# Performance work log

Measured on AMD Instinct MI355X. Metric: run time of the kernel, lower is better.

## Reference

```python
import jax, jax.numpy as jnp
import numpy as np

S, D = 4096, 512


def setup_inputs() -> dict:
    key = jax.random.key(0)
    ks = jax.random.split(key, 10)
    names = ['x', 'w_ql', 'w_kl', 'w_qr', 'w_kr', 'w_qg', 'w_kg', 'w_qloc', 'w_kloc', 'w_v']
    shapes = [(S, D)] + [(D, D)] * 9
    scale = [1.0] + [float(np.sqrt(2.0 / (D + D)))] * 9  # xavier-ish for weights
    return {n: jax.random.normal(k, sh, dtype=jnp.float32) * s
            for n, k, sh, s in zip(names, ks, shapes, scale)}


def reference(x, w_ql, w_kl, w_qr, w_kr, w_qg, w_kg, w_qloc, w_kloc, w_v):
    # x: [S, D]
    s, d = x.shape
    norm = jnp.sqrt(jnp.asarray(d, x.dtype))
    # strict upper triangle (j > i) is masked for the left boundary,
    # strict lower triangle (i > j) for the right boundary
    mask_up = jnp.triu(jnp.ones((s, s), dtype=bool), k=1)

    ql, kl = x @ w_ql, x @ w_kl
    qr, kr = x @ w_qr, x @ w_kr

    neg_inf = jnp.asarray(-jnp.inf, x.dtype)
    left_scores = jnp.where(mask_up, neg_inf, ql @ kl.T) / norm            # [S,S]
    left_boundary = jax.nn.softmax(left_scores, axis=1)
    right_scores = jnp.where(mask_up.T, neg_inf, qr @ kr.T) / norm
    right_boundary = jax.nn.softmax(right_scores, axis=1)

    # left_boundary @ triu(ones)  == forward cumsum along columns
    # right_boundary @ tril(ones) == reverse cumsum along columns
    left_cdf = jnp.cumsum(left_boundary, axis=1)
    right_cdf = jnp.cumsum(right_boundary[:, ::-1], axis=1)[:, ::-1]
    att_mask = left_cdf * right_cdf                                        # [S,S]

    s_glb = (x @ w_qg) @ (x @ w_kg).T                                      # [S,S]
    s_loc = ((x @ w_qloc) @ (x @ w_kloc).T) * att_mask                     # additive local path
    score = (s_glb + s_loc) / norm

    att_weight = jax.nn.softmax(score, axis=1)
    att_output = att_weight @ (x @ w_v)                                    # [S,D]
    return att_output, att_weight
```

## Files before the change

kernel.cpp:

```cpp
#include <hip/hip_runtime.h>


#define SS 4096
#define DD 512
#define INV_NORM 0.04419417382415922f

typedef _Float16 f16;
typedef f16 f16x8 __attribute__((ext_vector_type(8)));
typedef f16 f16x4 __attribute__((ext_vector_type(4)));
typedef float f32x4 __attribute__((ext_vector_type(4)));
typedef unsigned short ushort;
typedef ushort ushort4v __attribute__((ext_vector_type(4)));

#define GAS __attribute__((address_space(1)))
#define LAS __attribute__((address_space(3)))

#define BARM() asm volatile("s_barrier" ::: "memory")
#define WAITV(N) asm volatile("s_waitcnt vmcnt(" #N ")" ::: "memory")

__device__ __forceinline__ void ldsdma16(const void* g, void* l) {
  __builtin_amdgcn_global_load_lds((const GAS void*)g, (LAS void*)l, 16, 0, 0);
}

__device__ __forceinline__ ushort f2bf(float f) {
  unsigned u = __float_as_uint(f);
  return (ushort)((u + 0x7FFFu + ((u >> 16) & 1u)) >> 16);
}
__device__ __forceinline__ float bf2f(ushort h) {
  return __uint_as_float((unsigned)h << 16);
}

__device__ __forceinline__ void stage16(const f16* __restrict__ src, int ldk, f16* lds, int k0) {
  const int tid  = threadIdx.x;
  const int lane = tid & 63;
  const int wv   = tid >> 6;
  const int rb   = wv * 8 + (lane >> 3);
  const int cs   = lane & 7;
#pragma unroll
  for (int c = 0; c < 4; ++c) {
    const int r = c * 32 + rb;
    const int q = cs ^ (r & 7);
    ldsdma16(src + (size_t)r * ldk + k0 + q * 8, lds + c * 2048 + wv * 512);
  }
}

__device__ __forceinline__ f16x8 fragld(const f16* lds, int r0, int qb) {
  const int lane = threadIdx.x & 63;
  const int r = r0 + (lane & 15);
  const int q = (qb + (lane >> 4)) ^ (r & 7);
  return *(const f16x8*)(lds + r * 64 + q * 8);
}

__device__ __forceinline__ void mma64(const f16* As, const f16* Bs, f32x4 acc[2][8]) {
  const int wv = threadIdx.x >> 6;
#pragma unroll
  for (int ks = 0; ks < 2; ++ks) {
    const f16x8 a0 = fragld(As, wv * 32,      ks * 4);
    const f16x8 a1 = fragld(As, wv * 32 + 16, ks * 4);
#pragma unroll
    for (int j = 0; j < 8; ++j) {
      const f16x8 b = fragld(Bs, j * 16, ks * 4);
      acc[0][j] = __builtin_amdgcn_mfma_f32_16x16x32_f16(a0, b, acc[0][j], 0, 0, 0);
      acc[1][j] = __builtin_amdgcn_mfma_f32_16x16x32_f16(a1, b, acc[1][j], 0, 0, 0);
    }
  }
}

__global__ void k_cvt_x(const float* __restrict__ x, f16* __restrict__ xh) {
  const size_t i = ((size_t)blockIdx.x * 256 + threadIdx.x) * 4;
  const float4 f = *(const float4*)(x + i);
  f16x4 h = { (f16)f.x, (f16)f.y, (f16)f.z, (f16)f.w };
  *(f16x4*)(xh + i) = h;
}

__global__ void k_trw(const float* w0, const float* w1, const float* w2, const float* w3,
                      const float* w4, const float* w5, const float* w6, const float* w7,
                      const float* w8, f16* __restrict__ wt) {
  const float* srcs[9] = {w0, w1, w2, w3, w4, w5, w6, w7, w8};
  const float* src = srcs[blockIdx.z];
  f16* dst = wt + (size_t)blockIdx.z * DD * DD;
  __shared__ float t[32][33];
  const int n0 = blockIdx.x * 32, k0 = blockIdx.y * 32;
  const int tx = threadIdx.x, ty = threadIdx.y;
#pragma unroll
  for (int i = 0; i < 32; i += 8)
    t[ty + i][tx] = src[(size_t)(k0 + ty + i) * DD + n0 + tx];
  __syncthreads();
#pragma unroll
  for (int i = 0; i < 32; i += 8)
    dst[(size_t)(n0 + ty + i) * DD + k0 + tx] = (f16)t[tx][ty + i];
}

__global__ void k_trv(const f16* __restrict__ v, f16* __restrict__ vt) {
  __shared__ f16 t[32][33];
  const int n0 = blockIdx.x * 32, s0 = blockIdx.y * 32;
  const int tx = threadIdx.x, ty = threadIdx.y;
#pragma unroll
  for (int i = 0; i < 32; i += 8)
    t[ty + i][tx] = v[(size_t)(s0 + ty + i) * DD + n0 + tx];
  __syncthreads();
#pragma unroll
  for (int i = 0; i < 32; i += 8)
    vt[(size_t)(n0 + ty + i) * SS + s0 + tx] = t[tx][ty + i];
}

__global__ __launch_bounds__(256, 3) void k_proj(const f16* __restrict__ xh,
                                                 const f16* __restrict__ wt,
                                                 f16* __restrict__ proj) {
  __shared__ __align__(16) f16 As[8192];
  __shared__ __align__(16) f16 Bs[8192];
  const int z = blockIdx.z;
  const f16* B = wt + (size_t)z * DD * DD;
  f16* C = proj + (size_t)z * SS * DD;
  const int R0 = blockIdx.y * 128, C0 = blockIdx.x * 128;
  f32x4 acc[2][8];
#pragma unroll
  for (int i = 0; i < 2; ++i)
#pragma unroll
    for (int j = 0; j < 8; ++j) acc[i][j] = (f32x4){0.f, 0.f, 0.f, 0.f};
  for (int kb = 0; kb < DD / 64; ++kb) {
    __syncthreads();
    stage16(xh + (size_t)R0 * DD, DD, As, kb * 64);
    stage16(B  + (size_t)C0 * DD, DD, Bs, kb * 64);
    __syncthreads();
    mma64(As, Bs, acc);
  }
  const int lane = threadIdx.x & 63, wv = threadIdx.x >> 6;
  const int mm = lane & 15, quad = lane >> 4;
#pragma unroll
  for (int i = 0; i < 2; ++i)
#pragma unroll
    for (int j = 0; j < 8; ++j)
#pragma unroll
      for (int r = 0; r < 4; ++r)
        C[(size_t)(R0 + wv * 32 + i * 16 + quad * 4 + r) * DD + C0 + j * 16 + mm] =
            (f16)acc[i][j][r];
}

__global__ __launch_bounds__(256, 3) void k_bnd(const f16* __restrict__ proj,
                                                f16* __restrict__ eL,
                                                f16* __restrict__ eR) {
  const int t = blockIdx.x, dir = blockIdx.y;
  int rbk = (int)((sqrtf(8.f * t + 1.f) - 1.f) * 0.5f);
  while ((rbk + 1) * (rbk + 2) / 2 <= t) ++rbk;
  while (rbk * (rbk + 1) / 2 > t) --rbk;
  int jt = t - rbk * (rbk + 1) / 2;
  if (dir) { jt = 31 - jt; rbk = 31 - rbk; }
  __shared__ __align__(16) f16 As[8192];
  __shared__ __align__(16) f16 Bs[8192];
  const f16* q  = proj + (size_t)(dir ? 2 : 0) * SS * DD;
  const f16* kp = proj + (size_t)(dir ? 3 : 1) * SS * DD;
  const int R0 = rbk * 128, C0 = jt * 128;
  f32x4 acc[2][8];
#pragma unroll
  for (int i = 0; i < 2; ++i)
#pragma unroll
    for (int j = 0; j < 8; ++j) acc[i][j] = (f32x4){0.f, 0.f, 0.f, 0.f};
  for (int kb = 0; kb < DD / 64; ++kb) {
    __syncthreads();
    stage16(q  + (size_t)R0 * DD, DD, As, kb * 64);
    stage16(kp + (size_t)C0 * DD, DD, Bs, kb * 64);
    __syncthreads();
    mma64(As, Bs, acc);
  }
  const int lane = threadIdx.x & 63, wv = threadIdx.x >> 6;
  const int mm = lane & 15, quad = lane >> 4;
  const bool diag = (jt == rbk);
  f16* outp = dir ? eR : eL;
#pragma unroll
  for (int i = 0; i < 2; ++i)
#pragma unroll
    for (int r = 0; r < 4; ++r) {
      const int rl = wv * 32 + i * 16 + quad * 4 + r;
#pragma unroll
      for (int j = 0; j < 8; ++j) {
        const int cl = j * 16 + mm;
        const float sc = acc[i][j][r] * INV_NORM;
        const bool bad = diag && (dir ? (cl < rl) : (cl > rl));
        const float e = bad ? 0.f : __expf(sc);
        outp[(size_t)(R0 + rl) * SS + (C0 + cl)] = (f16)e;
      }
    }
}

__global__ __launch_bounds__(1024) void k_cumsum(f16* __restrict__ eL,
                                                 const f16* __restrict__ eR) {
  const int i = blockIdx.x;
  const int tid = threadIdx.x, lane = tid & 63, wv = tid >> 6;
  __shared__ float wsL[16], wsR[16];
  const int j0 = tid * 4;

  float pl[4] = {0.f, 0.f, 0.f, 0.f};
  if (j0 <= i) {
    const f16x4 hl = *(const f16x4*)(eL + (size_t)i * SS + j0);
#pragma unroll
    for (int u = 0; u < 4; ++u) pl[u] = (j0 + u <= i) ? (float)hl[u] : 0.f;
  }
#pragma unroll
  for (int u = 1; u < 4; ++u) pl[u] += pl[u - 1];
  const float Tl = pl[3];
  float sl = Tl;
#pragma unroll
  for (int d = 1; d < 64; d <<= 1) {
    const float o = __shfl_up(sl, (unsigned)d, 64);
    if (lane >= d) sl += o;
  }
  if (lane == 63) wsL[wv] = sl;

  float rr[4] = {0.f, 0.f, 0.f, 0.f}, pr[4];
  if (j0 + 3 >= i) {
    const f16x4 hr = *(const f16x4*)(eR + (size_t)i * SS + j0);
#pragma unroll
    for (int u = 0; u < 4; ++u) rr[u] = (j0 + u >= i) ? (float)hr[u] : 0.f;
  }
  pr[0] = rr[0];
#pragma unroll
  for (int u = 1; u < 4; ++u) pr[u] = pr[u - 1] + rr[u];
  const float Tr = pr[3];
  float sr = Tr;
#pragma unroll
  for (int d = 1; d < 64; d <<= 1) {
    const float o = __shfl_up(sr, (unsigned)d, 64);
    if (lane >= d) sr += o;
  }
  if (lane == 63) wsR[wv] = sr;

  __syncthreads();
  float offL = 0.f, totL = 0.f, offR = 0.f, totR = 0.f;
#pragma unroll
  for (int ww = 0; ww < 16; ++ww) {
    const float a = wsL[ww], b = wsR[ww];
    if (ww < wv) { offL += a; offR += b; }
    totL += a; totR += b;
  }
  const float exL = offL + sl - Tl;
  const float exR = offR + sr - Tr;
  const float invL = 1.f / totL, invR = 1.f / totR;

  f16x4 out;
#pragma unroll
  for (int u = 0; u < 4; ++u) {
    const int j = j0 + u;
    const float cdfL = (exL + pl[u]) * invL;
    const float pre  = exR + pr[u];
    const float cdfR = (totR - pre + rr[u]) * invR;
    const float m = (j < i) ? cdfL : ((j > i) ? cdfR : 1.f);
    out[u] = (f16)m;
  }
  *(f16x4*)(eL + (size_t)i * SS + j0) = out;
}

__device__ __forceinline__ float mask_ld(const f16* Am, const f16* Bm, int r, int c) {
  const f16* b = (c < 64) ? Am : Bm;
  const int cc = c & 63;
  const int q = (cc >> 3) ^ (r & 7);
  return (float)b[r * 64 + q * 8 + (cc & 7)];
}

__global__ __launch_bounds__(256, 2) void k_score(const f16* __restrict__ proj,
                                                  const f16* __restrict__ mask,
                                                  f16* __restrict__ ehalf,
                                                  float* __restrict__ lsc) {
  __shared__ __align__(16) f16 Ag[8192];
  __shared__ __align__(16) f16 Bg[8192];
  __shared__ __align__(16) f16 Al[8192];
  __shared__ __align__(16) f16 Bl[8192];
  const int jt = blockIdx.x, rbk = blockIdx.y;
  const f16* qg = proj + (size_t)4 * SS * DD;
  const f16* kg = proj + (size_t)5 * SS * DD;
  const f16* ql = proj + (size_t)6 * SS * DD;
  const f16* kl = proj + (size_t)7 * SS * DD;
  const int R0 = rbk * 128, C0 = jt * 128;
  f32x4 ag[2][8], al[2][8];
#pragma unroll
  for (int i = 0; i < 2; ++i)
#pragma unroll
    for (int j = 0; j < 8; ++j) {
      ag[i][j] = (f32x4){0.f, 0.f, 0.f, 0.f};
      al[i][j] = (f32x4){0.f, 0.f, 0.f, 0.f};
    }
  stage16(qg + (size_t)R0 * DD, DD, Ag, 0);
  stage16(kg + (size_t)C0 * DD, DD, Bg, 0);
  stage16(ql + (size_t)R0 * DD, DD, Al, 0);
  stage16(kl + (size_t)C0 * DD, DD, Bl, 0);
  for (int kb = 0; kb < DD / 64 - 1; ++kb) {
    WAITV(8);
    BARM();
    mma64(Ag, Bg, ag);
    BARM();
    stage16(qg + (size_t)R0 * DD, DD, Ag, kb * 64 + 64);
    stage16(kg + (size_t)C0 * DD, DD, Bg, kb * 64 + 64);
    WAITV(8);
    BARM();
    mma64(Al, Bl, al);
    BARM();
    stage16(ql + (size_t)R0 * DD, DD, Al, kb * 64 + 64);
    stage16(kl + (size_t)C0 * DD, DD, Bl, kb * 64 + 64);
  }
  WAITV(8);
  BARM();
  mma64(Ag, Bg, ag);
  BARM();
  stage16(mask + (size_t)R0 * SS, SS, Ag, C0);
  stage16(mask + (size_t)R0 * SS, SS, Bg, C0 + 64);
  WAITV(16);
  BARM();
  mma64(Al, Bl, al);
  WAITV(0);
  BARM();

  const int lane = threadIdx.x & 63, wv = threadIdx.x >> 6;
  const int mm = lane & 15, quad = lane >> 4;
  float ls[2][4];
#pragma unroll
  for (int i = 0; i < 2; ++i)
#pragma unroll
    for (int r = 0; r < 4; ++r) ls[i][r] = 0.f;
#pragma unroll
  for (int i = 0; i < 2; ++i)
#pragma unroll
    for (int r = 0; r < 4; ++r) {
      const int rl = wv * 32 + i * 16 + quad * 4 + r;
      const int rg = R0 + rl;
#pragma unroll
      for (int j = 0; j < 8; ++j) {
        const int cl = j * 16 + mm;
        const float mk = mask_ld(Ag, Bg, rl, cl);
        const float scv = (ag[i][j][r] + al[i][j][r] * mk) * INV_NORM;
        const float e = __expf(scv);
        ehalf[(size_t)rg * SS + (C0 + cl)] = (f16)e;
        ls[i][r] += e;
      }
    }
#pragma unroll
  for (int d = 1; d < 16; d <<= 1)
#pragma unroll
    for (int i = 0; i < 2; ++i)
#pragma unroll
      for (int r = 0; r < 4; ++r)
        ls[i][r] += __shfl_xor(ls[i][r], d, 64);
  if (mm == 0) {
#pragma unroll
    for (int i = 0; i < 2; ++i)
#pragma unroll
      for (int r = 0; r < 4; ++r)
        atomicAdd(&lsc[R0 + wv * 32 + i * 16 + quad * 4 + r], ls[i][r]);
  }
}

__global__ __launch_bounds__(256, 4) void k_pv(const f16* __restrict__ ehalf,
                                               const f16* __restrict__ vt,
                                               ushort* __restrict__ part) {
  __shared__ __align__(16) f16 As[8192];
  __shared__ __align__(16) f16 Bs[8192];
  const int C0 = blockIdx.x * 128, R0 = blockIdx.y * 128, zk = blockIdx.z;
  f32x4 acc[2][8];
#pragma unroll
  for (int i = 0; i < 2; ++i)
#pragma unroll
    for (int j = 0; j < 8; ++j) acc[i][j] = (f32x4){0.f, 0.f, 0.f, 0.f};
  for (int kb = 0; kb < 16; ++kb) {
    const int k0 = zk * 1024 + kb * 64;
    __syncthreads();
    stage16(ehalf + (size_t)R0 * SS, SS, As, k0);
    stage16(vt    + (size_t)C0 * SS, SS, Bs, k0);
    __syncthreads();
    mma64(As, Bs, acc);
  }
  const int lane = threadIdx.x & 63, wv = threadIdx.x >> 6;
  const int mm = lane & 15, quad = lane >> 4;
  ushort* P = part + (size_t)zk * SS * DD;
#pragma unroll
  for (int i = 0; i < 2; ++i)
#pragma unroll
    for (int j = 0; j < 8; ++j)
#pragma unroll
      for (int r = 0; r < 4; ++r)
        P[(size_t)(R0 + wv * 32 + i * 16 + quad * 4 + r) * DD + C0 + j * 16 + mm] =
            f2bf(acc[i][j][r]);
}

__global__ void k_fin(const f16* __restrict__ ehalf, const ushort* __restrict__ part,
                      const float* __restrict__ lsc, float* __restrict__ outw,
                      float* __restrict__ O) {
  const int bx = blockIdx.x;
  if (bx < 8192) {
    const size_t idx = ((size_t)bx * 256 + threadIdx.x) * 8;
    const int row = (int)(idx >> 12);
    const float inv = 1.f / lsc[row];
    const f16x8 h = *(const f16x8*)(ehalf + idx);
    float4 a = { (float)h[0] * inv, (float)h[1] * inv, (float)h[2] * inv, (float)h[3] * inv };
    float4 b = { (float)h[4] * inv, (float)h[5] * inv, (float)h[6] * inv, (float)h[7] * inv };
    *(float4*)(outw + idx) = a;
    *(float4*)(outw + idx + 4) = b;
  } else {
    const size_t idx = ((size_t)(bx - 8192) * 256 + threadIdx.x) * 4;
    const int row = (int)(idx >> 9);
    float s0 = 0.f, s1 = 0.f, s2 = 0.f, s3 = 0.f;
#pragma unroll
    for (int p = 0; p < 4; ++p) {
      const ushort4v v = *(const ushort4v*)(part + (size_t)p * SS * DD + idx);
      s0 += bf2f(v[0]); s1 += bf2f(v[1]); s2 += bf2f(v[2]); s3 += bf2f(v[3]);
    }
    const float inv = 1.f / lsc[row];
    float4 s = { s0 * inv, s1 * inv, s2 * inv, s3 * inv };
    *(float4*)(O + idx) = s;
  }
}

extern "C" void kernel_launch(void* const* d_in, const int* in_sizes, int n_in,
                              void* d_out, int out_size, void* d_ws, size_t ws_size,
                              hipStream_t stream) {
  (void)in_sizes; (void)n_in; (void)out_size; (void)ws_size;
  const float* x = (const float*)d_in[0];
  const float* w[9];
  for (int i = 0; i < 9; ++i) w[i] = (const float*)d_in[1 + i];
  float* O    = (float*)d_out;
  float* outw = O + (size_t)SS * DD;

  char* ws = (char*)d_ws;
  size_t off = 0;
  auto alloc = [&](size_t b) { void* p = ws + off; off += (b + 255) & ~(size_t)255; return p; };
  f16* xh     = (f16*)alloc((size_t)SS * DD * 2);
  f16* wt     = (f16*)alloc((size_t)9 * DD * DD * 2);
  f16* proj   = (f16*)alloc((size_t)9 * SS * DD * 2);
  f16* vt     = (f16*)alloc((size_t)DD * SS * 2);
  f16* eL     = (f16*)alloc((size_t)SS * SS * 2);
  f16* eR     = (f16*)alloc((size_t)SS * SS * 2);
  f16* ehalf  = (f16*)alloc((size_t)SS * SS * 2);
  float* lsc  = (float*)alloc((size_t)SS * 4);
  ushort* part = (ushort*)eR;

  hipMemsetAsync(lsc, 0, (size_t)SS * 4, stream);
  k_cvt_x<<<SS * DD / 1024, 256, 0, stream>>>(x, xh);
  k_trw<<<dim3(16, 16, 9), dim3(32, 8), 0, stream>>>(w[0], w[1], w[2], w[3], w[4],
                                                     w[5], w[6], w[7], w[8], wt);
  k_proj<<<dim3(4, 32, 9), 256, 0, stream>>>(xh, wt, proj);
  k_trv<<<dim3(16, 128), dim3(32, 8), 0, stream>>>(proj + (size_t)8 * SS * DD, vt);
  k_bnd<<<dim3(528, 2), 256, 0, stream>>>(proj, eL, eR);
  k_cumsum<<<SS, 1024, 0, stream>>>(eL, eR);
  k_score<<<dim3(32, 32), 256, 0, stream>>>(proj, eL, ehalf, lsc);
  k_pv<<<dim3(4, 32, 4), 256, 0, stream>>>(ehalf, vt, part);
  k_fin<<<10240, 256, 0, stream>>>(ehalf, part, lsc, outw, O);
}
```

Before: 290.6 us.

## Swizzle score block order, raise MFMA priority, halve PV column tile

The score kernel now remaps block indices so that consecutive workgroups land in different row and column tiles, aiming for better L2 reuse across XCDs. It raises wave priority around the MFMA sections and fixes the vmcnt wait before the last local-path MMA. The PV kernel moves from 128-column to 64-column tiles with a half-size B stage and a narrower MMA, doubling the grid for more parallelism. The narrower tile means each loaded ehalf tile is reused across fewer output columns, so A-side traffic rises.

```diff
diff --git a/kernel.cpp b/kernel.cpp
--- a/kernel.cpp
+++ b/kernel.cpp
@@ -44,6 +44,20 @@
   }
 }
 
+__device__ __forceinline__ void stage16h(const f16* __restrict__ src, int ldk, f16* lds, int k0) {
+  const int tid  = threadIdx.x;
+  const int lane = tid & 63;
+  const int wv   = tid >> 6;
+  const int rb   = wv * 8 + (lane >> 3);
+  const int cs   = lane & 7;
+#pragma unroll
+  for (int c = 0; c < 2; ++c) {
+    const int r = c * 32 + rb;
+    const int q = cs ^ (r & 7);
+    ldsdma16(src + (size_t)r * ldk + k0 + q * 8, lds + c * 2048 + wv * 512);
+  }
+}
+
 __device__ __forceinline__ f16x8 fragld(const f16* lds, int r0, int qb) {
   const int lane = threadIdx.x & 63;
   const int r = r0 + (lane & 15);
@@ -59,6 +73,21 @@
     const f16x8 a1 = fragld(As, wv * 32 + 16, ks * 4);
 #pragma unroll
     for (int j = 0; j < 8; ++j) {
+      const f16x8 b = fragld(Bs, j * 16, ks * 4);
+      acc[0][j] = __builtin_amdgcn_mfma_f32_16x16x32_f16(a0, b, acc[0][j], 0, 0, 0);
+      acc[1][j] = __builtin_amdgcn_mfma_f32_16x16x32_f16(a1, b, acc[1][j], 0, 0, 0);
+    }
+  }
+}
+
+__device__ __forceinline__ void mma3264(const f16* As, const f16* Bs, f32x4 acc[2][4]) {
+  const int wv = threadIdx.x >> 6;
+#pragma unroll
+  for (int ks = 0; ks < 2; ++ks) {
+    const f16x8 a0 = fragld(As, wv * 32,      ks * 4);
+    const f16x8 a1 = fragld(As, wv * 32 + 16, ks * 4);
+#pragma unroll
+    for (int j = 0; j < 4; ++j) {
       const f16x8 b = fragld(Bs, j * 16, ks * 4);
       acc[0][j] = __builtin_amdgcn_mfma_f32_16x16x32_f16(a0, b, acc[0][j], 0, 0, 0);
       acc[1][j] = __builtin_amdgcn_mfma_f32_16x16x32_f16(a1, b, acc[1][j], 0, 0, 0);
@@ -265,7 +294,9 @@
   __shared__ __align__(16) f16 Bg[8192];
   __shared__ __align__(16) f16 Al[8192];
   __shared__ __align__(16) f16 Bl[8192];
-  const int jt = blockIdx.x, rbk = blockIdx.y;
+  const int lin = blockIdx.y * 32 + blockIdx.x;
+  const int swz = (lin & 7) * 128 + (lin >> 3);
+  const int jt = swz & 31, rbk = swz >> 5;
   const f16* qg = proj + (size_t)4 * SS * DD;
   const f16* kg = proj + (size_t)5 * SS * DD;
   const f16* ql = proj + (size_t)6 * SS * DD;
@@ -286,26 +317,34 @@
   for (int kb = 0; kb < DD / 64 - 1; ++kb) {
     WAITV(8);
     BARM();
+    __builtin_amdgcn_s_setprio(1);
     mma64(Ag, Bg, ag);
+    __builtin_amdgcn_s_setprio(0);
     BARM();
     stage16(qg + (size_t)R0 * DD, DD, Ag, kb * 64 + 64);
     stage16(kg + (size_t)C0 * DD, DD, Bg, kb * 64 + 64);
     WAITV(8);
     BARM();
+    __builtin_amdgcn_s_setprio(1);
     mma64(Al, Bl, al);
+    __builtin_amdgcn_s_setprio(0);
     BARM();
     stage16(ql + (size_t)R0 * DD, DD, Al, kb * 64 + 64);
     stage16(kl + (size_t)C0 * DD, DD, Bl, kb * 64 + 64);
   }
   WAITV(8);
   BARM();
+  __builtin_amdgcn_s_setprio(1);
   mma64(Ag, Bg, ag);
+  __builtin_amdgcn_s_setprio(0);
   BARM();
   stage16(mask + (size_t)R0 * SS, SS, Ag, C0);
   stage16(mask + (size_t)R0 * SS, SS, Bg, C0 + 64);
-  WAITV(16);
+  WAITV(8);
   BARM();
+  __builtin_amdgcn_s_setprio(1);
   mma64(Al, Bl, al);
+  __builtin_amdgcn_s_setprio(0);
   WAITV(0);
   BARM();
 
@@ -352,20 +391,20 @@
                                                const f16* __restrict__ vt,
                                                ushort* __restrict__ part) {
   __shared__ __align__(16) f16 As[8192];
-  __shared__ __align__(16) f16 Bs[8192];
-  const int C0 = blockIdx.x * 128, R0 = blockIdx.y * 128, zk = blockIdx.z;
-  f32x4 acc[2][8];
-#pragma unroll
-  for (int i = 0; i < 2; ++i)
-#pragma unroll
-    for (int j = 0; j < 8; ++j) acc[i][j] = (f32x4){0.f, 0.f, 0.f, 0.f};
+  __shared__ __align__(16) f16 Bs[4096];
+  const int C0 = blockIdx.x * 64, R0 = blockIdx.y * 128, zk = blockIdx.z;
+  f32x4 acc[2][4];
+#pragma unroll
+  for (int i = 0; i < 2; ++i)
+#pragma unroll
+    for (int j = 0; j < 4; ++j) acc[i][j] = (f32x4){0.f, 0.f, 0.f, 0.f};
   for (int kb = 0; kb < 16; ++kb) {
     const int k0 = zk * 1024 + kb * 64;
     __syncthreads();
-    stage16(ehalf + (size_t)R0 * SS, SS, As, k0);
-    stage16(vt    + (size_t)C0 * SS, SS, Bs, k0);
-    __syncthreads();
-    mma64(As, Bs, acc);
+    stage16 (ehalf + (size_t)R0 * SS, SS, As, k0);
+    stage16h(vt    + (size_t)C0 * SS, SS, Bs, k0);
+    __syncthreads();
+    mma3264(As, Bs, acc);
   }
   const int lane = threadIdx.x & 63, wv = threadIdx.x >> 6;
   const int mm = lane & 15, quad = lane >> 4;
@@ -373,7 +412,7 @@
 #pragma unroll
   for (int i = 0; i < 2; ++i)
 #pragma unroll
-    for (int j = 0; j < 8; ++j)
+    for (int j = 0; j < 4; ++j)
 #pragma unroll
       for (int r = 0; r < 4; ++r)
         P[(size_t)(R0 + wv * 32 + i * 16 + quad * 4 + r) * DD + C0 + j * 16 + mm] =
@@ -440,6 +479,6 @@
   k_bnd<<<dim3(528, 2), 256, 0, stream>>>(proj, eL, eR);
   k_cumsum<<<SS, 1024, 0, stream>>>(eL, eR);
   k_score<<<dim3(32, 32), 256, 0, stream>>>(proj, eL, ehalf, lsc);
-  k_pv<<<dim3(4, 32, 4), 256, 0, stream>>>(ehalf, vt, part);
+  k_pv<<<dim3(8, 32, 4), 256, 0, stream>>>(ehalf, vt, part);
   k_fin<<<10240, 256, 0, stream>>>(ehalf, part, lsc, outw, O);
 }
```

Measured after the change: 312.7 us. 7.6% more time.

## Merge prep kernels, fuse V transpose into projection, prioritize MFMA in score loop

Applied to the files above, without the earlier changes.

Combines the x conversion and weight transpose kernels into one launch. The V transpose kernel is removed: the projection kernel now writes the transposed V directly from its accumulators when z==8. In the score kernel the MFMA sections are wrapped in s_setprio raises and one vmcnt wait is tightened from 16 to 8. This cuts launch overhead and one extra pass over V, at the cost of strided uncoalesced stores for vt in the projection epilogue.

```diff
diff --git a/kernel.cpp b/kernel.cpp
--- a/kernel.cpp
+++ b/kernel.cpp
@@ -66,22 +66,27 @@
   }
 }
 
-__global__ void k_cvt_x(const float* __restrict__ x, f16* __restrict__ xh) {
-  const size_t i = ((size_t)blockIdx.x * 256 + threadIdx.x) * 4;
-  const float4 f = *(const float4*)(x + i);
-  f16x4 h = { (f16)f.x, (f16)f.y, (f16)f.z, (f16)f.w };
-  *(f16x4*)(xh + i) = h;
-}
-
-__global__ void k_trw(const float* w0, const float* w1, const float* w2, const float* w3,
-                      const float* w4, const float* w5, const float* w6, const float* w7,
-                      const float* w8, f16* __restrict__ wt) {
+__global__ void k_prep(const float* __restrict__ x, const float* w0, const float* w1,
+                       const float* w2, const float* w3, const float* w4, const float* w5,
+                       const float* w6, const float* w7, const float* w8,
+                       f16* __restrict__ xh, f16* __restrict__ wt) {
+  const int bx = blockIdx.x;
+  if (bx < 2048) {
+    const size_t i = ((size_t)bx * 256 + threadIdx.x) * 4;
+    const float4 f = *(const float4*)(x + i);
+    f16x4 h = { (f16)f.x, (f16)f.y, (f16)f.z, (f16)f.w };
+    *(f16x4*)(xh + i) = h;
+    return;
+  }
+  const int idx = bx - 2048;
+  const int bz = idx >> 8;
+  const int rem = idx & 255;
+  const int n0 = (rem & 15) * 32, k0 = (rem >> 4) * 32;
   const float* srcs[9] = {w0, w1, w2, w3, w4, w5, w6, w7, w8};
-  const float* src = srcs[blockIdx.z];
-  f16* dst = wt + (size_t)blockIdx.z * DD * DD;
+  const float* src = srcs[bz];
+  f16* dst = wt + (size_t)bz * DD * DD;
   __shared__ float t[32][33];
-  const int n0 = blockIdx.x * 32, k0 = blockIdx.y * 32;
-  const int tx = threadIdx.x, ty = threadIdx.y;
+  const int tx = threadIdx.x & 31, ty = threadIdx.x >> 5;
 #pragma unroll
   for (int i = 0; i < 32; i += 8)
     t[ty + i][tx] = src[(size_t)(k0 + ty + i) * DD + n0 + tx];
@@ -91,22 +96,10 @@
     dst[(size_t)(n0 + ty + i) * DD + k0 + tx] = (f16)t[tx][ty + i];
 }
 
-__global__ void k_trv(const f16* __restrict__ v, f16* __restrict__ vt) {
-  __shared__ f16 t[32][33];
-  const int n0 = blockIdx.x * 32, s0 = blockIdx.y * 32;
-  const int tx = threadIdx.x, ty = threadIdx.y;
-#pragma unroll
-  for (int i = 0; i < 32; i += 8)
-    t[ty + i][tx] = v[(size_t)(s0 + ty + i) * DD + n0 + tx];
-  __syncthreads();
-#pragma unroll
-  for (int i = 0; i < 32; i += 8)
-    vt[(size_t)(n0 + ty + i) * SS + s0 + tx] = t[tx][ty + i];
-}
-
 __global__ __launch_bounds__(256, 3) void k_proj(const f16* __restrict__ xh,
                                                  const f16* __restrict__ wt,
-                                                 f16* __restrict__ proj) {
+                                                 f16* __restrict__ proj,
+                                                 f16* __restrict__ vt) {
   __shared__ __align__(16) f16 As[8192];
   __shared__ __align__(16) f16 Bs[8192];
   const int z = blockIdx.z;
@@ -135,6 +128,16 @@
       for (int r = 0; r < 4; ++r)
         C[(size_t)(R0 + wv * 32 + i * 16 + quad * 4 + r) * DD + C0 + j * 16 + mm] =
             (f16)acc[i][j][r];
+  if (z == 8) {
+#pragma unroll
+    for (int i = 0; i < 2; ++i)
+#pragma unroll
+      for (int j = 0; j < 8; ++j)
+#pragma unroll
+        for (int r = 0; r < 4; ++r)
+          vt[(size_t)(C0 + j * 16 + mm) * SS + (R0 + wv * 32 + i * 16 + quad * 4 + r)] =
+              (f16)acc[i][j][r];
+  }
 }
 
 __global__ __launch_bounds__(256, 3) void k_bnd(const f16* __restrict__ proj,
@@ -286,26 +289,34 @@
   for (int kb = 0; kb < DD / 64 - 1; ++kb) {
     WAITV(8);
     BARM();
+    __builtin_amdgcn_s_setprio(1);
     mma64(Ag, Bg, ag);
+    __builtin_amdgcn_s_setprio(0);
     BARM();
     stage16(qg + (size_t)R0 * DD, DD, Ag, kb * 64 + 64);
     stage16(kg + (size_t)C0 * DD, DD, Bg, kb * 64 + 64);
     WAITV(8);
     BARM();
+    __builtin_amdgcn_s_setprio(1);
     mma64(Al, Bl, al);
+    __builtin_amdgcn_s_setprio(0);
     BARM();
     stage16(ql + (size_t)R0 * DD, DD, Al, kb * 64 + 64);
     stage16(kl + (size_t)C0 * DD, DD, Bl, kb * 64 + 64);
   }
   WAITV(8);
   BARM();
+  __builtin_amdgcn_s_setprio(1);
   mma64(Ag, Bg, ag);
+  __builtin_amdgcn_s_setprio(0);
   BARM();
   stage16(mask + (size_t)R0 * SS, SS, Ag, C0);
   stage16(mask + (size_t)R0 * SS, SS, Bg, C0 + 64);
-  WAITV(16);
+  WAITV(8);
   BARM();
+  __builtin_amdgcn_s_setprio(1);
   mma64(Al, Bl, al);
+  __builtin_amdgcn_s_setprio(0);
   WAITV(0);
   BARM();
 
@@ -432,11 +443,9 @@
   ushort* part = (ushort*)eR;
 
   hipMemsetAsync(lsc, 0, (size_t)SS * 4, stream);
-  k_cvt_x<<<SS * DD / 1024, 256, 0, stream>>>(x, xh);
-  k_trw<<<dim3(16, 16, 9), dim3(32, 8), 0, stream>>>(w[0], w[1], w[2], w[3], w[4],
-                                                     w[5], w[6], w[7], w[8], wt);
-  k_proj<<<dim3(4, 32, 9), 256, 0, stream>>>(xh, wt, proj);
-  k_trv<<<dim3(16, 128), dim3(32, 8), 0, stream>>>(proj + (size_t)8 * SS * DD, vt);
+  k_prep<<<4352, 256, 0, stream>>>(x, w[0], w[1], w[2], w[3], w[4], w[5], w[6], w[7], w[8],
+                                   xh, wt);
+  k_proj<<<dim3(4, 32, 9), 256, 0, stream>>>(xh, wt, proj, vt);
   k_bnd<<<dim3(528, 2), 256, 0, stream>>>(proj, eL, eR);
   k_cumsum<<<SS, 1024, 0, stream>>>(eL, eR);
   k_score<<<dim3(32, 32), 256, 0, stream>>>(proj, eL, ehalf, lsc);
```

Measured after the change: 290.0 us. No clear change (-0.2%).
